# Kernel optimization log

Hardware: AMD Instinct MI355X
Metric: run time of the kernel (lower is better)

The kernel has to match this reference:

```python
import jax, jax.numpy as jnp
import numpy as np

N_HEAD = 4
D_MODEL = 256
FEAT_DIM = 256
D_K = D_MODEL // N_HEAD  # 64
TEMP = float(np.sqrt(D_K))
LN_EPS = 1e-5


def setup_inputs() -> dict:
    key = jax.random.key(0)
    ks = jax.random.split(key, 12)
    B, N_src, N_ngh = 2048, 1, 128
    src = jax.random.normal(ks[0], (B, N_src, FEAT_DIM), dtype=jnp.float32)
    seq = jax.random.normal(ks[1], (B, N_ngh, FEAT_DIM), dtype=jnp.float32)
    mask = jax.random.randint(ks[2], (B, N_ngh), 0, 2) > 0
    s_qk = np.sqrt(2.0 / (D_MODEL + D_K))
    w_qs = jax.random.normal(ks[3], (N_HEAD * D_K, D_MODEL), dtype=jnp.float32) * s_qk
    w_ks = jax.random.normal(ks[4], (N_HEAD * D_K, D_MODEL), dtype=jnp.float32) * s_qk
    w_vs = jax.random.normal(ks[5], (N_HEAD * D_K, D_MODEL), dtype=jnp.float32) * s_qk
    fc_w = jax.random.normal(ks[6], (D_MODEL, N_HEAD * D_K), dtype=jnp.float32) * 0.05
    fc_b = jnp.zeros((D_MODEL,), dtype=jnp.float32)
    ln_g = jnp.ones((D_MODEL,), dtype=jnp.float32)
    ln_b = jnp.zeros((D_MODEL,), dtype=jnp.float32)
    fc1_w = jax.random.normal(ks[7], (FEAT_DIM, 2 * D_MODEL), dtype=jnp.float32) * 0.05
    fc1_b = jnp.zeros((FEAT_DIM,), dtype=jnp.float32)
    fc2_w = jax.random.normal(ks[8], (FEAT_DIM, FEAT_DIM), dtype=jnp.float32) * 0.05
    fc2_b = jnp.zeros((FEAT_DIM,), dtype=jnp.float32)
    return {"src": src, "seq": seq, "mask": mask, "w_qs": w_qs, "w_ks": w_ks,
            "w_vs": w_vs, "fc_w": fc_w, "fc_b": fc_b, "ln_g": ln_g, "ln_b": ln_b,
            "fc1_w": fc1_w, "fc1_b": fc1_b, "fc2_w": fc2_w, "fc2_b": fc2_b}


def _forward(src, seq, mask, w_qs, w_ks, w_vs, fc_w, fc_b, ln_g, ln_b,
             fc1_w, fc1_b, fc2_w, fc2_b):
    B, N_src, _ = src.shape
    N_ngh = seq.shape[1]
    nn_ = N_ngh // N_src
    # projections (dropout is identity in eval mode)
    qh = (src @ w_qs.T).reshape(B, N_src, N_HEAD, D_K)              # bshd
    kh = (seq @ w_ks.T).reshape(B, N_src, nn_, N_HEAD, D_K)        # bsnhd
    vh = (seq @ w_vs.T).reshape(B, N_src, nn_, N_HEAD, D_K)
    scores = jnp.einsum('bshd,bsnhd->bshn', qh, kh) / TEMP          # [B,Ns,H,nn]
    # Replicate original mask layout exactly: attn rows are flat in (b,s,h)
    # order, but mask was built with .repeat(n_head,1,1) -> head-major tiling.
    flat = scores.reshape(B * N_src * N_HEAD, nn_)
    mask_rep = jnp.tile(mask.reshape(B * N_src, nn_), (N_HEAD, 1))  # [H*B*Ns, nn]
    flat = jnp.where(mask_rep, -1e10, flat)
    attn = jax.nn.softmax(flat, axis=-1).reshape(B, N_src, N_HEAD, nn_)
    out = jnp.einsum('bshn,bsnhd->bshd', attn, vh).reshape(B, N_src, N_HEAD * D_K)
    out = out @ fc_w.T + fc_b
    x = out + src  # residual (q == src since pos_dim == 0)
    mu = jnp.mean(x, axis=-1, keepdims=True)
    var = jnp.mean(jnp.square(x - mu), axis=-1, keepdims=True)
    x = (x - mu) * jax.lax.rsqrt(var + LN_EPS) * ln_g + ln_b
    # MergeLayer (non_linear=True)
    h = jax.nn.relu(jnp.concatenate([x, src], axis=-1) @ fc1_w.T + fc1_b)
    z = h @ fc2_w.T + fc2_b                                        # [B,Ns,feat]
    return z, attn


def reference(src, seq, mask, w_qs, w_ks, w_vs, fc_w, fc_b, ln_g, ln_b,
              fc1_w, fc1_b, fc2_w, fc2_b):
    return _forward(src, seq, mask, w_qs, w_ks, w_vs, fc_w, fc_b, ln_g, ln_b,
                    fc1_w, fc1_b, fc2_w, fc2_b)
```

## Files before the change

kernel.cpp:

```cpp
#include <hip/hip_runtime.h>

typedef unsigned int uint32;
typedef unsigned short ushort16;

#define DI __device__ __forceinline__

#define BATCH 2048
#define NN    128
#define DM    256
#define NH    4
#define DK    64

DI float bf2f(ushort16 h) { return __uint_as_float(((uint32)h) << 16); }

DI ushort16 f2bf(float f) {
    uint32 u = __float_as_uint(f);
    uint32 r = u + 0x7fffu + ((u >> 16) & 1u);
    return (ushort16)(r >> 16);
}

DI void unpack8(const uint4 v, float f[8]) {
    f[0] = __uint_as_float(v.x << 16);
    f[1] = __uint_as_float(v.x & 0xffff0000u);
    f[2] = __uint_as_float(v.y << 16);
    f[3] = __uint_as_float(v.y & 0xffff0000u);
    f[4] = __uint_as_float(v.z << 16);
    f[5] = __uint_as_float(v.z & 0xffff0000u);
    f[6] = __uint_as_float(v.w << 16);
    f[7] = __uint_as_float(v.w & 0xffff0000u);
}

DI float dot8(const float* a, const float f[8], float acc) {
    acc = fmaf(a[0], f[0], acc);
    acc = fmaf(a[1], f[1], acc);
    acc = fmaf(a[2], f[2], acc);
    acc = fmaf(a[3], f[3], acc);
    acc = fmaf(a[4], f[4], acc);
    acc = fmaf(a[5], f[5], acc);
    acc = fmaf(a[6], f[6], acc);
    acc = fmaf(a[7], f[7], acc);
    return acc;
}

#define WOFF_QS  0
#define WOFF_KS  65536
#define WOFF_VS  131072
#define WOFF_FC  196608
#define WOFF_FC1 262144
#define WOFF_FC2 393216

__global__ __launch_bounds__(256) void prep_kernel(
    const float* __restrict__ wqs, const float* __restrict__ wks,
    const float* __restrict__ wvs, const float* __restrict__ fcw,
    const float* __restrict__ fc1w, const float* __restrict__ fc2w,
    ushort16* __restrict__ out)
{
    const int bid = blockIdx.x;
    const float* srcp; size_t soff, doff;
    if (bid < 64)       { srcp = wqs;  soff = (size_t)bid * 1024;         doff = WOFF_QS;  }
    else if (bid < 128) { srcp = wks;  soff = (size_t)(bid - 64) * 1024;  doff = WOFF_KS;  }
    else if (bid < 192) { srcp = wvs;  soff = (size_t)(bid - 128) * 1024; doff = WOFF_VS;  }
    else if (bid < 256) { srcp = fcw;  soff = (size_t)(bid - 192) * 1024; doff = WOFF_FC;  }
    else if (bid < 384) { srcp = fc1w; soff = (size_t)(bid - 256) * 1024; doff = WOFF_FC1; }
    else                { srcp = fc2w; soff = (size_t)(bid - 384) * 1024; doff = WOFF_FC2; }
    const int t = threadIdx.x;
    float4 v = *(const float4*)(srcp + soff + t * 4);
    uint2 pk;
    pk.x = (uint32)f2bf(v.x) | ((uint32)f2bf(v.y) << 16);
    pk.y = (uint32)f2bf(v.z) | ((uint32)f2bf(v.w) << 16);
    *(uint2*)(out + doff + soff + t * 4) = pk;
}

__global__ __launch_bounds__(256) void qu_kernel(
    const float* __restrict__ src, const ushort16* __restrict__ wbf,
    float* __restrict__ u)
{
    __shared__ float sS[8][DM];
    __shared__ float sQ[8][DM];
    const int t  = threadIdx.x;
    const int b0 = blockIdx.x * 8;

    #pragma unroll
    for (int r = 0; r < 8; ++r) sS[r][t] = src[(size_t)(b0 + r) * DM + t];
    __syncthreads();

    {
        float acc[8] = {0.f,0.f,0.f,0.f,0.f,0.f,0.f,0.f};
        const ushort16* wrow = wbf + WOFF_QS + (size_t)t * DM;
        for (int kc = 0; kc < DM; kc += 8) {
            uint4 w8 = *(const uint4*)(wrow + kc);
            float wf[8]; unpack8(w8, wf);
            #pragma unroll
            for (int r = 0; r < 8; ++r) acc[r] = dot8(&sS[r][kc], wf, acc[r]);
        }
        #pragma unroll
        for (int r = 0; r < 8; ++r) sQ[r][t] = acc[r];
    }
    __syncthreads();

    const ushort16* wks = wbf + WOFF_KS;
    for (int h = 0; h < NH; ++h) {
        float ua[8] = {0.f,0.f,0.f,0.f,0.f,0.f,0.f,0.f};
        for (int dc = 0; dc < DK; dc += 8) {
            float wv[8];
            #pragma unroll
            for (int e = 0; e < 8; ++e)
                wv[e] = bf2f(wks[(size_t)(h * DK + dc + e) * DM + t]);
            #pragma unroll
            for (int r = 0; r < 8; ++r) {
                float4 qa = *(const float4*)&sQ[r][h * DK + dc];
                float4 qb = *(const float4*)&sQ[r][h * DK + dc + 4];
                float a = ua[r];
                a = fmaf(qa.x, wv[0], a); a = fmaf(qa.y, wv[1], a);
                a = fmaf(qa.z, wv[2], a); a = fmaf(qa.w, wv[3], a);
                a = fmaf(qb.x, wv[4], a); a = fmaf(qb.y, wv[5], a);
                a = fmaf(qb.z, wv[6], a); a = fmaf(qb.w, wv[7], a);
                ua[r] = a;
            }
        }
        #pragma unroll
        for (int r = 0; r < 8; ++r)
            u[(size_t)(b0 + r) * (NH * DM) + h * DM + t] = ua[r] * 0.125f;
    }
}

#define SEQ_STRIDE 264
#define U_STRIDE   264

__global__ __launch_bounds__(256) void attn_kernel(
    const float* __restrict__ seq, const int* __restrict__ mask,
    const float* __restrict__ u, float* __restrict__ c,
    float* __restrict__ attn_out)
{
    __shared__ ushort16 sseq[NN * SEQ_STRIDE];
    __shared__ float    sbuf[2048];
    __shared__ float    sattn[NN * NH];

    const int t = threadIdx.x;
    const int b = blockIdx.x;

    #pragma unroll
    for (int i = 0; i < 4; ++i)
        sbuf[i * U_STRIDE + t] = u[(size_t)b * 1024 + i * 256 + t];

    const float* sp = seq + (size_t)b * (NN * DM);
    #pragma unroll
    for (int it = 0; it < 32; ++it) {
        int idx = it * 1024 + t * 4;
        int row = idx >> 8, col = idx & 255;
        float4 v = *(const float4*)(sp + idx);
        uint2 pk;
        pk.x = (uint32)f2bf(v.x) | ((uint32)f2bf(v.y) << 16);
        pk.y = (uint32)f2bf(v.z) | ((uint32)f2bf(v.w) << 16);
        *(uint2*)&sseq[row * SEQ_STRIDE + col] = pk;
    }
    __syncthreads();

    {
        const int h  = t & 3;
        const int n0 = t >> 2;
        const float* uh = &sbuf[h * U_STRIDE];
        const ushort16* r0 = &sseq[n0 * SEQ_STRIDE];
        const ushort16* r1 = &sseq[(n0 + 64) * SEQ_STRIDE];
        float s0 = 0.f, s1 = 0.f;
        for (int kc = 0; kc < DM; kc += 8) {
            uint4 va = *(const uint4*)(r0 + kc);
            uint4 vb = *(const uint4*)(r1 + kc);
            float fa[8], fb[8];
            unpack8(va, fa); unpack8(vb, fb);
            s0 = dot8(&uh[kc], fa, s0);
            s1 = dot8(&uh[kc], fb, s1);
        }
        int mr = (4 * b + h) & (BATCH - 1);
        if (mask[(size_t)mr * NN + n0] != 0)      s0 = -1e10f;
        if (mask[(size_t)mr * NN + n0 + 64] != 0) s1 = -1e10f;
        sattn[n0 * 4 + h]        = s0;
        sattn[(n0 + 64) * 4 + h] = s1;
    }
    __syncthreads();

    {
        const int w = t >> 6, l = t & 63;
        float x0 = sattn[l * 4 + w], x1 = sattn[(l + 64) * 4 + w];
        float mx = fmaxf(x0, x1);
        #pragma unroll
        for (int o = 32; o > 0; o >>= 1) mx = fmaxf(mx, __shfl_xor(mx, o, 64));
        float e0 = __expf(x0 - mx), e1 = __expf(x1 - mx);
        float sm = e0 + e1;
        #pragma unroll
        for (int o = 32; o > 0; o >>= 1) sm += __shfl_xor(sm, o, 64);
        float inv = 1.f / sm;
        float a0 = e0 * inv, a1 = e1 * inv;
        sattn[l * 4 + w]        = a0;
        sattn[(l + 64) * 4 + w] = a1;
        attn_out[(size_t)b * (NH * NN) + w * NN + l]      = a0;
        attn_out[(size_t)b * (NH * NN) + w * NN + l + 64] = a1;
    }
    __syncthreads();

    {
        const int ng = t >> 7;
        const int jp = t & 127;
        float cc[4][2] = {{0.f,0.f},{0.f,0.f},{0.f,0.f},{0.f,0.f}};
        for (int i = 0; i < 64; ++i) {
            int n = ng * 64 + i;
            uint32 v = *(const uint32*)&sseq[n * SEQ_STRIDE + jp * 2];
            float f0 = __uint_as_float(v << 16);
            float f1 = __uint_as_float(v & 0xffff0000u);
            float4 at = *(const float4*)&sattn[n * 4];
            cc[0][0] = fmaf(at.x, f0, cc[0][0]); cc[0][1] = fmaf(at.x, f1, cc[0][1]);
            cc[1][0] = fmaf(at.y, f0, cc[1][0]); cc[1][1] = fmaf(at.y, f1, cc[1][1]);
            cc[2][0] = fmaf(at.z, f0, cc[2][0]); cc[2][1] = fmaf(at.z, f1, cc[2][1]);
            cc[3][0] = fmaf(at.w, f0, cc[3][0]); cc[3][1] = fmaf(at.w, f1, cc[3][1]);
        }
        __syncthreads();
        #pragma unroll
        for (int h = 0; h < 4; ++h) {
            sbuf[ng * 1024 + h * 256 + jp * 2]     = cc[h][0];
            sbuf[ng * 1024 + h * 256 + jp * 2 + 1] = cc[h][1];
        }
    }
    __syncthreads();
    #pragma unroll
    for (int h = 0; h < 4; ++h)
        c[(size_t)b * 1024 + h * 256 + t] = sbuf[h * 256 + t] + sbuf[1024 + h * 256 + t];
}

__global__ __launch_bounds__(256) void mlp_kernel(
    const float* __restrict__ c, const float* __restrict__ src,
    const ushort16* __restrict__ wbf,
    const float* __restrict__ fcb, const float* __restrict__ lng,
    const float* __restrict__ lnb, const float* __restrict__ fc1b,
    const float* __restrict__ fc2b, float* __restrict__ zout)
{
    __shared__ float sC[8][1024];
    __shared__ float sA[8][256];
    __shared__ float sX[8][256];
    __shared__ float sS[8][256];
    __shared__ float sH[8][256];
    __shared__ float sRed[4][8][2];

    const int t  = threadIdx.x;
    const int b0 = blockIdx.x * 8;
    const int h  = t >> 6;

    #pragma unroll
    for (int i = 0; i < 8; ++i)
        *(float4*)&sC[i][t * 4] = *(const float4*)&c[(size_t)(b0 + i) * 1024 + t * 4];
    #pragma unroll
    for (int r = 0; r < 8; ++r) sS[r][t] = src[(size_t)(b0 + r) * DM + t];
    __syncthreads();

    {
        float acc[8] = {0.f,0.f,0.f,0.f,0.f,0.f,0.f,0.f};
        const ushort16* wr = wbf + WOFF_VS + (size_t)t * DM;
        for (int kc = 0; kc < DM; kc += 8) {
            uint4 w8 = *(const uint4*)(wr + kc);
            float wf[8]; unpack8(w8, wf);
            #pragma unroll
            for (int r = 0; r < 8; ++r) acc[r] = dot8(&sC[r][h * 256 + kc], wf, acc[r]);
        }
        #pragma unroll
        for (int r = 0; r < 8; ++r) sA[r][t] = acc[r];
    }
    __syncthreads();

    float xv[8];
    {
        float acc[8] = {0.f,0.f,0.f,0.f,0.f,0.f,0.f,0.f};
        const ushort16* wr = wbf + WOFF_FC + (size_t)t * DM;
        for (int kc = 0; kc < DM; kc += 8) {
            uint4 w8 = *(const uint4*)(wr + kc);
            float wf[8]; unpack8(w8, wf);
            #pragma unroll
            for (int r = 0; r < 8; ++r) acc[r] = dot8(&sA[r][kc], wf, acc[r]);
        }
        float bb = fcb[t];
        #pragma unroll
        for (int r = 0; r < 8; ++r) xv[r] = acc[r] + bb + sS[r][t];
    }
    {
        const int w = t >> 6, l = t & 63;
        #pragma unroll
        for (int r = 0; r < 8; ++r) {
            float vs = xv[r], vq = xv[r] * xv[r];
            #pragma unroll
            for (int o = 32; o > 0; o >>= 1) {
                vs += __shfl_xor(vs, o, 64);
                vq += __shfl_xor(vq, o, 64);
            }
            if (l == 0) { sRed[w][r][0] = vs; sRed[w][r][1] = vq; }
        }
        __syncthreads();
        float g = lng[t], bb = lnb[t];
        #pragma unroll
        for (int r = 0; r < 8; ++r) {
            float S = sRed[0][r][0] + sRed[1][r][0] + sRed[2][r][0] + sRed[3][r][0];
            float Q = sRed[0][r][1] + sRed[1][r][1] + sRed[2][r][1] + sRed[3][r][1];
            float mu  = S * (1.f / 256.f);
            float var = Q * (1.f / 256.f) - mu * mu;
            float rs  = rsqrtf(var + 1e-5f);
            sX[r][t] = (xv[r] - mu) * rs * g + bb;
        }
    }
    __syncthreads();

    {
        float acc[8] = {0.f,0.f,0.f,0.f,0.f,0.f,0.f,0.f};
        const ushort16* wr = wbf + WOFF_FC1 + (size_t)t * 512;
        for (int kc = 0; kc < 256; kc += 8) {
            uint4 w8 = *(const uint4*)(wr + kc);
            float wf[8]; unpack8(w8, wf);
            #pragma unroll
            for (int r = 0; r < 8; ++r) acc[r] = dot8(&sX[r][kc], wf, acc[r]);
        }
        for (int kc = 0; kc < 256; kc += 8) {
            uint4 w8 = *(const uint4*)(wr + 256 + kc);
            float wf[8]; unpack8(w8, wf);
            #pragma unroll
            for (int r = 0; r < 8; ++r) acc[r] = dot8(&sS[r][kc], wf, acc[r]);
        }
        float bb = fc1b[t];
        #pragma unroll
        for (int r = 0; r < 8; ++r) sH[r][t] = fmaxf(acc[r] + bb, 0.f);
    }
    __syncthreads();

    {
        float acc[8] = {0.f,0.f,0.f,0.f,0.f,0.f,0.f,0.f};
        const ushort16* wr = wbf + WOFF_FC2 + (size_t)t * DM;
        for (int kc = 0; kc < DM; kc += 8) {
            uint4 w8 = *(const uint4*)(wr + kc);
            float wf[8]; unpack8(w8, wf);
            #pragma unroll
            for (int r = 0; r < 8; ++r) acc[r] = dot8(&sH[r][kc], wf, acc[r]);
        }
        float bb = fc2b[t];
        #pragma unroll
        for (int r = 0; r < 8; ++r)
            zout[(size_t)(b0 + r) * DM + t] = acc[r] + bb;
    }
}

extern "C" void kernel_launch(void* const* d_in, const int* in_sizes, int n_in,
                              void* d_out, int out_size, void* d_ws, size_t ws_size,
                              hipStream_t stream)
{
    const float* src  = (const float*)d_in[0];
    const float* seq  = (const float*)d_in[1];
    const int*   mask = (const int*)d_in[2];
    const float* wqs  = (const float*)d_in[3];
    const float* wks  = (const float*)d_in[4];
    const float* wvs  = (const float*)d_in[5];
    const float* fcw  = (const float*)d_in[6];
    const float* fcb  = (const float*)d_in[7];
    const float* lng  = (const float*)d_in[8];
    const float* lnb  = (const float*)d_in[9];
    const float* fc1w = (const float*)d_in[10];
    const float* fc1b = (const float*)d_in[11];
    const float* fc2w = (const float*)d_in[12];
    const float* fc2b = (const float*)d_in[13];

    float* zout     = (float*)d_out;
    float* attn_out = zout + (size_t)BATCH * DM;

    float* u = (float*)d_ws;
    float* cbuf = u + (size_t)BATCH * 1024;
    ushort16* wbf = (ushort16*)(cbuf + (size_t)BATCH * 1024);

    prep_kernel<<<448, 256, 0, stream>>>(wqs, wks, wvs, fcw, fc1w, fc2w, wbf);
    qu_kernel<<<256, 256, 0, stream>>>(src, wbf, u);
    attn_kernel<<<BATCH, 256, 0, stream>>>(seq, mask, u, cbuf, attn_out);
    mlp_kernel<<<256, 256, 0, stream>>>(cbuf, src, wbf, fcb, lng, lnb,
                                        fc1b, fc2b, zout);
}
```

Baseline: 472.2 us.

## Read seq directly from global in attention, transpose K weights, halve rows per block

The attention kernel no longer stages the 128x256 seq tile into shared memory as bf16. The score and context loops now read fp32 seq straight from global memory, which frees shared memory so more blocks can be resident per CU. The K-weight prep kernel writes a transposed copy so the u computation in qu_kernel can use vectorized row loads instead of strided scalar loads. qu_kernel and mlp_kernel now process 4 rows per block with twice as many blocks, and the context reduction is split four ways. The trade-off is that seq is read from global twice (scores, then context) and relies on cache hits, and weight reuse per block is lower.

```diff
diff --git a/kernel.cpp b/kernel.cpp
--- a/kernel.cpp
+++ b/kernel.cpp
@@ -56,14 +56,23 @@
     ushort16* __restrict__ out)
 {
     const int bid = blockIdx.x;
+    const int t   = threadIdx.x;
+    if (bid >= 64 && bid < 128) {
+        int base = (bid - 64) * 1024 + t * 4;
+        float4 v = *(const float4*)(wks + base);
+        int r = base >> 8, c = base & 255;
+        out[WOFF_KS + (size_t)(c + 0) * 256 + r] = f2bf(v.x);
+        out[WOFF_KS + (size_t)(c + 1) * 256 + r] = f2bf(v.y);
+        out[WOFF_KS + (size_t)(c + 2) * 256 + r] = f2bf(v.z);
+        out[WOFF_KS + (size_t)(c + 3) * 256 + r] = f2bf(v.w);
+        return;
+    }
     const float* srcp; size_t soff, doff;
     if (bid < 64)       { srcp = wqs;  soff = (size_t)bid * 1024;         doff = WOFF_QS;  }
-    else if (bid < 128) { srcp = wks;  soff = (size_t)(bid - 64) * 1024;  doff = WOFF_KS;  }
     else if (bid < 192) { srcp = wvs;  soff = (size_t)(bid - 128) * 1024; doff = WOFF_VS;  }
     else if (bid < 256) { srcp = fcw;  soff = (size_t)(bid - 192) * 1024; doff = WOFF_FC;  }
     else if (bid < 384) { srcp = fc1w; soff = (size_t)(bid - 256) * 1024; doff = WOFF_FC1; }
     else                { srcp = fc2w; soff = (size_t)(bid - 384) * 1024; doff = WOFF_FC2; }
-    const int t = threadIdx.x;
     float4 v = *(const float4*)(srcp + soff + t * 4);
     uint2 pk;
     pk.x = (uint32)f2bf(v.x) | ((uint32)f2bf(v.y) << 16);
@@ -75,101 +84,89 @@
     const float* __restrict__ src, const ushort16* __restrict__ wbf,
     float* __restrict__ u)
 {
-    __shared__ float sS[8][DM];
-    __shared__ float sQ[8][DM];
+    __shared__ float sS[4][DM];
+    __shared__ float sQ[4][DM];
     const int t  = threadIdx.x;
-    const int b0 = blockIdx.x * 8;
-
-    #pragma unroll
-    for (int r = 0; r < 8; ++r) sS[r][t] = src[(size_t)(b0 + r) * DM + t];
-    __syncthreads();
-
-    {
-        float acc[8] = {0.f,0.f,0.f,0.f,0.f,0.f,0.f,0.f};
+    const int b0 = blockIdx.x * 4;
+
+    #pragma unroll
+    for (int r = 0; r < 4; ++r) sS[r][t] = src[(size_t)(b0 + r) * DM + t];
+    __syncthreads();
+
+    {
+        float acc[4] = {0.f,0.f,0.f,0.f};
         const ushort16* wrow = wbf + WOFF_QS + (size_t)t * DM;
+        #pragma unroll 2
         for (int kc = 0; kc < DM; kc += 8) {
             uint4 w8 = *(const uint4*)(wrow + kc);
             float wf[8]; unpack8(w8, wf);
             #pragma unroll
-            for (int r = 0; r < 8; ++r) acc[r] = dot8(&sS[r][kc], wf, acc[r]);
-        }
-        #pragma unroll
-        for (int r = 0; r < 8; ++r) sQ[r][t] = acc[r];
-    }
-    __syncthreads();
-
-    const ushort16* wks = wbf + WOFF_KS;
+            for (int r = 0; r < 4; ++r) acc[r] = dot8(&sS[r][kc], wf, acc[r]);
+        }
+        #pragma unroll
+        for (int r = 0; r < 4; ++r) sQ[r][t] = acc[r];
+    }
+    __syncthreads();
+
+    const ushort16* wr2 = wbf + WOFF_KS + (size_t)t * DM;
+    #pragma unroll
     for (int h = 0; h < NH; ++h) {
-        float ua[8] = {0.f,0.f,0.f,0.f,0.f,0.f,0.f,0.f};
+        float ua[4] = {0.f,0.f,0.f,0.f};
+        #pragma unroll 2
         for (int dc = 0; dc < DK; dc += 8) {
-            float wv[8];
-            #pragma unroll
-            for (int e = 0; e < 8; ++e)
-                wv[e] = bf2f(wks[(size_t)(h * DK + dc + e) * DM + t]);
-            #pragma unroll
-            for (int r = 0; r < 8; ++r) {
-                float4 qa = *(const float4*)&sQ[r][h * DK + dc];
-                float4 qb = *(const float4*)&sQ[r][h * DK + dc + 4];
-                float a = ua[r];
-                a = fmaf(qa.x, wv[0], a); a = fmaf(qa.y, wv[1], a);
-                a = fmaf(qa.z, wv[2], a); a = fmaf(qa.w, wv[3], a);
-                a = fmaf(qb.x, wv[4], a); a = fmaf(qb.y, wv[5], a);
-                a = fmaf(qb.z, wv[6], a); a = fmaf(qb.w, wv[7], a);
-                ua[r] = a;
-            }
-        }
-        #pragma unroll
-        for (int r = 0; r < 8; ++r)
+            uint4 w8 = *(const uint4*)(wr2 + h * DK + dc);
+            float wf[8]; unpack8(w8, wf);
+            #pragma unroll
+            for (int r = 0; r < 4; ++r) ua[r] = dot8(&sQ[r][h * DK + dc], wf, ua[r]);
+        }
+        #pragma unroll
+        for (int r = 0; r < 4; ++r)
             u[(size_t)(b0 + r) * (NH * DM) + h * DM + t] = ua[r] * 0.125f;
     }
 }
 
-#define SEQ_STRIDE 264
-#define U_STRIDE   264
+#define U_STRIDE 264
 
 __global__ __launch_bounds__(256) void attn_kernel(
     const float* __restrict__ seq, const int* __restrict__ mask,
     const float* __restrict__ u, float* __restrict__ c,
     float* __restrict__ attn_out)
 {
-    __shared__ ushort16 sseq[NN * SEQ_STRIDE];
-    __shared__ float    sbuf[2048];
-    __shared__ float    sattn[NN * NH];
+    __shared__ float sred[4096];
+    __shared__ float sattn[NN * NH];
 
     const int t = threadIdx.x;
     const int b = blockIdx.x;
+    const float* sp = seq + (size_t)b * (NN * DM);
 
     #pragma unroll
     for (int i = 0; i < 4; ++i)
-        sbuf[i * U_STRIDE + t] = u[(size_t)b * 1024 + i * 256 + t];
-
-    const float* sp = seq + (size_t)b * (NN * DM);
-    #pragma unroll
-    for (int it = 0; it < 32; ++it) {
-        int idx = it * 1024 + t * 4;
-        int row = idx >> 8, col = idx & 255;
-        float4 v = *(const float4*)(sp + idx);
-        uint2 pk;
-        pk.x = (uint32)f2bf(v.x) | ((uint32)f2bf(v.y) << 16);
-        pk.y = (uint32)f2bf(v.z) | ((uint32)f2bf(v.w) << 16);
-        *(uint2*)&sseq[row * SEQ_STRIDE + col] = pk;
-    }
+        sred[i * U_STRIDE + t] = u[(size_t)b * 1024 + i * 256 + t];
     __syncthreads();
 
     {
         const int h  = t & 3;
         const int n0 = t >> 2;
-        const float* uh = &sbuf[h * U_STRIDE];
-        const ushort16* r0 = &sseq[n0 * SEQ_STRIDE];
-        const ushort16* r1 = &sseq[(n0 + 64) * SEQ_STRIDE];
+        const float* uh = &sred[h * U_STRIDE];
+        const float* r0 = sp + n0 * DM;
+        const float* r1 = r0 + 64 * DM;
         float s0 = 0.f, s1 = 0.f;
-        for (int kc = 0; kc < DM; kc += 8) {
-            uint4 va = *(const uint4*)(r0 + kc);
-            uint4 vb = *(const uint4*)(r1 + kc);
-            float fa[8], fb[8];
-            unpack8(va, fa); unpack8(vb, fb);
-            s0 = dot8(&uh[kc], fa, s0);
-            s1 = dot8(&uh[kc], fb, s1);
+        #pragma unroll 2
+        for (int kc = 0; kc < DM; kc += 8) {
+            float4 u0 = *(const float4*)(uh + kc);
+            float4 u1 = *(const float4*)(uh + kc + 4);
+            float4 a0 = *(const float4*)(r0 + kc);
+            float4 a1 = *(const float4*)(r0 + kc + 4);
+            float4 d0 = *(const float4*)(r1 + kc);
+            float4 d1 = *(const float4*)(r1 + kc + 4);
+            s0 = fmaf(u0.x, a0.x, s0); s0 = fmaf(u0.y, a0.y, s0);
+            s0 = fmaf(u0.z, a0.z, s0); s0 = fmaf(u0.w, a0.w, s0);
+            s0 = fmaf(u1.x, a1.x, s0); s0 = fmaf(u1.y, a1.y, s0);
+            s0 = fmaf(u1.z, a1.z, s0); s0 = fmaf(u1.w, a1.w, s0);
+            s1 = fmaf(u0.x, d0.x, s1); s1 = fmaf(u0.y, d0.y, s1);
+            s1 = fmaf(u0.z, d0.z, s1); s1 = fmaf(u0.w, d0.w, s1);
+            s1 = fmaf(u1.x, d1.x, s1); s1 = fmaf(u1.y, d1.y, s1);
+            s1 = fmaf(u1.z, d1.z, s1); s1 = fmaf(u1.w, d1.w, s1);
         }
         int mr = (4 * b + h) & (BATCH - 1);
         if (mask[(size_t)mr * NN + n0] != 0)      s0 = -1e10f;
@@ -199,31 +196,38 @@
     __syncthreads();
 
     {
-        const int ng = t >> 7;
-        const int jp = t & 127;
-        float cc[4][2] = {{0.f,0.f},{0.f,0.f},{0.f,0.f},{0.f,0.f}};
-        for (int i = 0; i < 64; ++i) {
-            int n = ng * 64 + i;
-            uint32 v = *(const uint32*)&sseq[n * SEQ_STRIDE + jp * 2];
-            float f0 = __uint_as_float(v << 16);
-            float f1 = __uint_as_float(v & 0xffff0000u);
+        const int q  = t >> 6;
+        const int j4 = (t & 63) * 4;
+        float cc[4][4];
+        #pragma unroll
+        for (int h2 = 0; h2 < 4; ++h2) {
+            cc[h2][0] = 0.f; cc[h2][1] = 0.f; cc[h2][2] = 0.f; cc[h2][3] = 0.f;
+        }
+        #pragma unroll 2
+        for (int i = 0; i < 32; ++i) {
+            const int n = q * 32 + i;
+            float4 sv = *(const float4*)(sp + n * DM + j4);
             float4 at = *(const float4*)&sattn[n * 4];
-            cc[0][0] = fmaf(at.x, f0, cc[0][0]); cc[0][1] = fmaf(at.x, f1, cc[0][1]);
-            cc[1][0] = fmaf(at.y, f0, cc[1][0]); cc[1][1] = fmaf(at.y, f1, cc[1][1]);
-            cc[2][0] = fmaf(at.z, f0, cc[2][0]); cc[2][1] = fmaf(at.z, f1, cc[2][1]);
-            cc[3][0] = fmaf(at.w, f0, cc[3][0]); cc[3][1] = fmaf(at.w, f1, cc[3][1]);
-        }
-        __syncthreads();
-        #pragma unroll
-        for (int h = 0; h < 4; ++h) {
-            sbuf[ng * 1024 + h * 256 + jp * 2]     = cc[h][0];
-            sbuf[ng * 1024 + h * 256 + jp * 2 + 1] = cc[h][1];
-        }
-    }
-    __syncthreads();
-    #pragma unroll
-    for (int h = 0; h < 4; ++h)
-        c[(size_t)b * 1024 + h * 256 + t] = sbuf[h * 256 + t] + sbuf[1024 + h * 256 + t];
+            cc[0][0] = fmaf(at.x, sv.x, cc[0][0]); cc[0][1] = fmaf(at.x, sv.y, cc[0][1]);
+            cc[0][2] = fmaf(at.x, sv.z, cc[0][2]); cc[0][3] = fmaf(at.x, sv.w, cc[0][3]);
+            cc[1][0] = fmaf(at.y, sv.x, cc[1][0]); cc[1][1] = fmaf(at.y, sv.y, cc[1][1]);
+            cc[1][2] = fmaf(at.y, sv.z, cc[1][2]); cc[1][3] = fmaf(at.y, sv.w, cc[1][3]);
+            cc[2][0] = fmaf(at.z, sv.x, cc[2][0]); cc[2][1] = fmaf(at.z, sv.y, cc[2][1]);
+            cc[2][2] = fmaf(at.z, sv.z, cc[2][2]); cc[2][3] = fmaf(at.z, sv.w, cc[2][3]);
+            cc[3][0] = fmaf(at.w, sv.x, cc[3][0]); cc[3][1] = fmaf(at.w, sv.y, cc[3][1]);
+            cc[3][2] = fmaf(at.w, sv.z, cc[3][2]); cc[3][3] = fmaf(at.w, sv.w, cc[3][3]);
+        }
+        #pragma unroll
+        for (int h2 = 0; h2 < 4; ++h2)
+            *(float4*)&sred[q * 1024 + h2 * 256 + j4] =
+                make_float4(cc[h2][0], cc[h2][1], cc[h2][2], cc[h2][3]);
+    }
+    __syncthreads();
+    #pragma unroll
+    for (int h2 = 0; h2 < 4; ++h2)
+        c[(size_t)b * 1024 + h2 * 256 + t] =
+            sred[h2 * 256 + t] + sred[1024 + h2 * 256 + t] +
+            sred[2048 + h2 * 256 + t] + sred[3072 + h2 * 256 + t];
 }
 
 __global__ __launch_bounds__(256) void mlp_kernel(
@@ -233,56 +237,58 @@
     const float* __restrict__ lnb, const float* __restrict__ fc1b,
     const float* __restrict__ fc2b, float* __restrict__ zout)
 {
-    __shared__ float sC[8][1024];
-    __shared__ float sA[8][256];
-    __shared__ float sX[8][256];
-    __shared__ float sS[8][256];
-    __shared__ float sH[8][256];
-    __shared__ float sRed[4][8][2];
+    __shared__ float sC[4][1024];
+    __shared__ float sA[4][256];
+    __shared__ float sX[4][256];
+    __shared__ float sS[4][256];
+    __shared__ float sH[4][256];
+    __shared__ float sRed[4][4][2];
 
     const int t  = threadIdx.x;
-    const int b0 = blockIdx.x * 8;
+    const int b0 = blockIdx.x * 4;
     const int h  = t >> 6;
 
     #pragma unroll
-    for (int i = 0; i < 8; ++i)
+    for (int i = 0; i < 4; ++i)
         *(float4*)&sC[i][t * 4] = *(const float4*)&c[(size_t)(b0 + i) * 1024 + t * 4];
     #pragma unroll
-    for (int r = 0; r < 8; ++r) sS[r][t] = src[(size_t)(b0 + r) * DM + t];
-    __syncthreads();
-
-    {
-        float acc[8] = {0.f,0.f,0.f,0.f,0.f,0.f,0.f,0.f};
+    for (int r = 0; r < 4; ++r) sS[r][t] = src[(size_t)(b0 + r) * DM + t];
+    __syncthreads();
+
+    {
+        float acc[4] = {0.f,0.f,0.f,0.f};
         const ushort16* wr = wbf + WOFF_VS + (size_t)t * DM;
+        #pragma unroll 2
         for (int kc = 0; kc < DM; kc += 8) {
             uint4 w8 = *(const uint4*)(wr + kc);
             float wf[8]; unpack8(w8, wf);
             #pragma unroll
-            for (int r = 0; r < 8; ++r) acc[r] = dot8(&sC[r][h * 256 + kc], wf, acc[r]);
-        }
-        #pragma unroll
-        for (int r = 0; r < 8; ++r) sA[r][t] = acc[r];
-    }
-    __syncthreads();
-
-    float xv[8];
-    {
-        float acc[8] = {0.f,0.f,0.f,0.f,0.f,0.f,0.f,0.f};
+            for (int r = 0; r < 4; ++r) acc[r] = dot8(&sC[r][h * 256 + kc], wf, acc[r]);
+        }
+        #pragma unroll
+        for (int r = 0; r < 4; ++r) sA[r][t] = acc[r];
+    }
+    __syncthreads();
+
+    float xv[4];
+    {
+        float acc[4] = {0.f,0.f,0.f,0.f};
         const ushort16* wr = wbf + WOFF_FC + (size_t)t * DM;
+        #pragma unroll 2
         for (int kc = 0; kc < DM; kc += 8) {
             uint4 w8 = *(const uint4*)(wr + kc);
             float wf[8]; unpack8(w8, wf);
             #pragma unroll
-            for (int r = 0; r < 8; ++r) acc[r] = dot8(&sA[r][kc], wf, acc[r]);
+            for (int r = 0; r < 4; ++r) acc[r] = dot8(&sA[r][kc], wf, acc[r]);
         }
         float bb = fcb[t];
         #pragma unroll
-        for (int r = 0; r < 8; ++r) xv[r] = acc[r] + bb + sS[r][t];
+        for (int r = 0; r < 4; ++r) xv[r] = acc[r] + bb + sS[r][t];
     }
     {
         const int w = t >> 6, l = t & 63;
         #pragma unroll
-        for (int r = 0; r < 8; ++r) {
+        for (int r = 0; r < 4; ++r) {
             float vs = xv[r], vq = xv[r] * xv[r];
             #pragma unroll
             for (int o = 32; o > 0; o >>= 1) {
@@ -294,7 +300,7 @@
         __syncthreads();
         float g = lng[t], bb = lnb[t];
         #pragma unroll
-        for (int r = 0; r < 8; ++r) {
+        for (int r = 0; r < 4; ++r) {
             float S = sRed[0][r][0] + sRed[1][r][0] + sRed[2][r][0] + sRed[3][r][0];
             float Q = sRed[0][r][1] + sRed[1][r][1] + sRed[2][r][1] + sRed[3][r][1];
             float mu  = S * (1.f / 256.f);
@@ -306,38 +312,41 @@
     __syncthreads();
 
     {
-        float acc[8] = {0.f,0.f,0.f,0.f,0.f,0.f,0.f,0.f};
+        float acc[4] = {0.f,0.f,0.f,0.f};
         const ushort16* wr = wbf + WOFF_FC1 + (size_t)t * 512;
+        #pragma unroll 2
         for (int kc = 0; kc < 256; kc += 8) {
             uint4 w8 = *(const uint4*)(wr + kc);
             float wf[8]; unpack8(w8, wf);
             #pragma unroll
-            for (int r = 0; r < 8; ++r) acc[r] = dot8(&sX[r][kc], wf, acc[r]);
-        }
+            for (int r = 0; r < 4; ++r) acc[r] = dot8(&sX[r][kc], wf, acc[r]);
+        }
+        #pragma unroll 2
         for (int kc = 0; kc < 256; kc += 8) {
             uint4 w8 = *(const uint4*)(wr + 256 + kc);
             float wf[8]; unpack8(w8, wf);
             #pragma unroll
-            for (int r = 0; r < 8; ++r) acc[r] = dot8(&sS[r][kc], wf, acc[r]);
+            for (int r = 0; r < 4; ++r) acc[r] = dot8(&sS[r][kc], wf, acc[r]);
         }
         float bb = fc1b[t];
         #pragma unroll
-        for (int r = 0; r < 8; ++r) sH[r][t] = fmaxf(acc[r] + bb, 0.f);
-    }
-    __syncthreads();
-
-    {
-        float acc[8] = {0.f,0.f,0.f,0.f,0.f,0.f,0.f,0.f};
+        for (int r = 0; r < 4; ++r) sH[r][t] = fmaxf(acc[r] + bb, 0.f);
+    }
+    __syncthreads();
+
+    {
+        float acc[4] = {0.f,0.f,0.f,0.f};
         const ushort16* wr = wbf + WOFF_FC2 + (size_t)t * DM;
+        #pragma unroll 2
         for (int kc = 0; kc < DM; kc += 8) {
             uint4 w8 = *(const uint4*)(wr + kc);
             float wf[8]; unpack8(w8, wf);
             #pragma unroll
-            for (int r = 0; r < 8; ++r) acc[r] = dot8(&sH[r][kc], wf, acc[r]);
+            for (int r = 0; r < 4; ++r) acc[r] = dot8(&sH[r][kc], wf, acc[r]);
         }
         float bb = fc2b[t];
         #pragma unroll
-        for (int r = 0; r < 8; ++r)
+        for (int r = 0; r < 4; ++r)
             zout[(size_t)(b0 + r) * DM + t] = acc[r] + bb;
     }
 }
@@ -369,8 +378,8 @@
     ushort16* wbf = (ushort16*)(cbuf + (size_t)BATCH * 1024);
 
     prep_kernel<<<448, 256, 0, stream>>>(wqs, wks, wvs, fcw, fc1w, fc2w, wbf);
-    qu_kernel<<<256, 256, 0, stream>>>(src, wbf, u);
+    qu_kernel<<<512, 256, 0, stream>>>(src, wbf, u);
     attn_kernel<<<BATCH, 256, 0, stream>>>(seq, mask, u, cbuf, attn_out);
-    mlp_kernel<<<256, 256, 0, stream>>>(cbuf, src, wbf, fcb, lng, lnb,
+    mlp_kernel<<<512, 256, 0, stream>>>(cbuf, src, wbf, fcb, lng, lnb,
                                         fc1b, fc2b, zout);
 }
```

Result: slower. 483.0 us (+2.3%).
